# Kernel optimization log

Hardware: AMD Instinct MI355X
Metric: run time of the kernel (lower is better)

The kernel has to match this reference:

```python
import jax, jax.numpy as jnp
import numpy as np
from functools import partial

VOCAB, EMB = 32000, 512
HIDDEN = (1024, 512, 256)
OUT = 7
S, T = 1024, 64  # S = scan (seq) axis, T = 'timesteps' (effective batch)


def _lstm_layer(x, Wih, Whh, bih, bhh):
    """PyTorch-semantics LSTM over axis 0. x: (S, B, E) -> hs: (S, B, H)."""
    B = x.shape[1]
    H = Whh.shape[1]
    # precompute input contribution to all gates: (S, B, 4H)
    xg = jnp.einsum('sbe,ge->sbg', x, Wih) + bih + bhh

    def step(carry, xg_t):
        h, c = carry
        gates = xg_t + h @ Whh.T  # (B, 4H)
        i, f, g, o = jnp.split(gates, 4, axis=-1)  # torch gate order i,f,g,o
        i = jax.nn.sigmoid(i)
        f = jax.nn.sigmoid(f)
        g = jnp.tanh(g)
        o = jax.nn.sigmoid(o)
        c = f * c + i * g
        h = o * jnp.tanh(c)
        return (h, c), h

    init = (jnp.zeros((B, H), x.dtype), jnp.zeros((B, H), x.dtype))
    _, hs = jax.lax.scan(step, init, xg)
    return hs


def setup_inputs():
    key = jax.random.key(0)
    ks = jax.random.split(key, 16)
    inp = {
        'tokens': jax.random.randint(ks[0], (S, T), 0, VOCAB),
        'emb': jax.random.normal(ks[1], (VOCAB, EMB), jnp.float32) * 0.02,
    }
    dims = [(EMB, HIDDEN[0]), (HIDDEN[0], HIDDEN[1]), (HIDDEN[1], HIDDEN[2])]
    for li, (e, h) in enumerate(dims):
        s = 1.0 / np.sqrt(h)
        inp[f'Wih{li}'] = jax.random.uniform(ks[2 + 4 * li], (4 * h, e), jnp.float32, -s, s)
        inp[f'Whh{li}'] = jax.random.uniform(ks[3 + 4 * li], (4 * h, h), jnp.float32, -s, s)
        inp[f'bih{li}'] = jax.random.uniform(ks[4 + 4 * li], (4 * h,), jnp.float32, -s, s)
        inp[f'bhh{li}'] = jax.random.uniform(ks[5 + 4 * li], (4 * h,), jnp.float32, -s, s)
    s = 1.0 / np.sqrt(HIDDEN[2])
    inp['Wlin'] = jax.random.uniform(ks[14], (OUT, HIDDEN[2]), jnp.float32, -s, s)
    inp['blin'] = jax.random.uniform(ks[15], (OUT,), jnp.float32, -s, s)
    return inp


def reference(tokens, emb, Wih0, Whh0, bih0, bhh0, Wih1, Whh1, bih1, bhh1,
              Wih2, Whh2, bih2, bhh2, Wlin, blin):
    x = emb[tokens]                                  # (S, T, EMB)
    h = _lstm_layer(x, Wih0, Whh0, bih0, bhh0)       # (S, T, 1024)
    h = _lstm_layer(h, Wih1, Whh1, bih1, bhh1)       # (S, T, 512)
    h = _lstm_layer(h, Wih2, Whh2, bih2, bhh2)       # (S, T, 256)
    last = h[:, T - 1, :]                            # out[:, timesteps-1, :]
    out = last @ Wlin.T + blin                       # (S, OUT); dropout is identity in eval
    return out
```

## Files before the change

### kernel.cpp

```cpp
#include <hip/hip_runtime.h>
#include <math.h>

#define SLEN 1024

__device__ __forceinline__ float sigf(float x) { return 1.0f / (1.0f + __expf(-x)); }

__device__ __forceinline__ float agent_ld(const float* p) {
  return __hip_atomic_load(p, __ATOMIC_RELAXED, __HIP_MEMORY_SCOPE_AGENT);
}
__device__ __forceinline__ void agent_st(float* p, float v) {
  __hip_atomic_store(p, v, __ATOMIC_RELAXED, __HIP_MEMORY_SCOPE_AGENT);
}
__device__ __forceinline__ bool is_sent(float f) { return __float_as_uint(f) == 0xFFFFFFFFu; }

__device__ __forceinline__ void pin4(float4& v) {
  asm volatile("" : "+v"(v.x), "+v"(v.y), "+v"(v.z), "+v"(v.w));
}

__global__ void embed_k(const int* __restrict__ tokens, const float* __restrict__ emb,
                        float* __restrict__ x) {
  const int t = blockIdx.x;
  const int tok = tokens[t * 64 + 63];
  const float4 v = ((const float4*)(emb + (size_t)tok * 512))[threadIdx.x];
  ((float4*)(x + (size_t)t * 512))[threadIdx.x] = v;
}

template<int HOUT, int EIN, bool POLL_IN>
__device__ void lstm_role(int ublk,
                          const float* __restrict__ Wih, const float* __restrict__ Whh,
                          const float* __restrict__ bih, const float* __restrict__ bhh,
                          const float* __restrict__ in_hist, float* __restrict__ hout) {
  constexpr int C     = EIN + HOUT;
  constexpr int SLOTS = C / 256;
  constexpr int XQ    = EIN / 4;
  constexpr int EPN   = EIN / 512;
  constexpr int HPN   = (HOUT >= 512) ? (HOUT / 512) : 1;
  constexpr bool HGUARD = (HOUT < 512);

  __shared__ __align__(16) float in_lds[2][C];
  __shared__ float h_g[8];

  const int tid = threadIdx.x;
  const int c   = tid & 63;
  const int w   = tid >> 6;
  const int u0  = ublk * 8;
  const int u   = u0 + w;

  float4 wreg[4][SLOTS];
  #pragma unroll
  for (int g = 0; g < 4; ++g) {
    const size_t grow = (size_t)g * HOUT + (size_t)u;
    const float4* wih4 = (const float4*)(Wih + grow * EIN);
    const float4* whh4 = (const float4*)(Whh + grow * HOUT);
    #pragma unroll
    for (int s = 0; s < SLOTS; ++s) {
      const int c4 = s * 64 + c;
      wreg[g][s] = (c4 < XQ) ? wih4[c4] : whh4[c4 - XQ];
    }
  }
  #pragma unroll
  for (int g = 0; g < 4; ++g)
    #pragma unroll
    for (int s = 0; s < SLOTS; ++s)
      pin4(wreg[g][s]);

  float bg0 = 0.f, bg1 = 0.f, bg2 = 0.f, bg3 = 0.f, cst = 0.f;
  if (c == 0) {
    bg0 = bih[0*HOUT + u] + bhh[0*HOUT + u];
    bg1 = bih[1*HOUT + u] + bhh[1*HOUT + u];
    bg2 = bih[2*HOUT + u] + bhh[2*HOUT + u];
    bg3 = bih[3*HOUT + u] + bhh[3*HOUT + u];
  }

  for (int t = 0; t < SLEN; ++t) {
    float ev[EPN];
    float hv[HPN];
    const float* esrc = in_hist + (size_t)t * EIN + EPN * tid;
    const float* hsrc = hout + (size_t)((t > 0 ? t : 1) - 1) * HOUT + HPN * tid;
    const bool hon   = (!HGUARD) || (tid * HPN < HOUT);
    const bool hneed = (t > 0) && hon;

    if constexpr (POLL_IN) {
      for (;;) {
        bool ok = true;
        #pragma unroll
        for (int i = 0; i < EPN; ++i) ev[i] = agent_ld(esrc + i);
        if (hneed) {
          #pragma unroll
          for (int i = 0; i < HPN; ++i) hv[i] = agent_ld(hsrc + i);
          #pragma unroll
          for (int i = 0; i < HPN; ++i) ok &= !is_sent(hv[i]);
        }
        #pragma unroll
        for (int i = 0; i < EPN; ++i) ok &= !is_sent(ev[i]);
        if (ok) break;
        __builtin_amdgcn_s_sleep(1);
      }
    } else {
      #pragma unroll
      for (int i = 0; i < EPN; ++i) ev[i] = esrc[i];
      if (hneed) {
        for (;;) {
          bool ok = true;
          #pragma unroll
          for (int i = 0; i < HPN; ++i) hv[i] = agent_ld(hsrc + i);
          #pragma unroll
          for (int i = 0; i < HPN; ++i) ok &= !is_sent(hv[i]);
          if (ok) break;
          __builtin_amdgcn_s_sleep(1);
        }
      }
    }

    float* dst = in_lds[t & 1];
    #pragma unroll
    for (int i = 0; i < EPN; ++i) dst[EPN * tid + i] = ev[i];
    if (hon) {
      #pragma unroll
      for (int i = 0; i < HPN; ++i) dst[EIN + HPN * tid + i] = hneed ? hv[i] : 0.0f;
    }
    __syncthreads();

    float a0 = 0.f, a1 = 0.f, a2 = 0.f, a3 = 0.f;
    const float4* iv4 = (const float4*)dst;
    #pragma unroll
    for (int s = 0; s < SLOTS; ++s) {
      const float4 iv = iv4[s * 64 + c];
      a0 += wreg[0][s].x*iv.x + wreg[0][s].y*iv.y + wreg[0][s].z*iv.z + wreg[0][s].w*iv.w;
      a1 += wreg[1][s].x*iv.x + wreg[1][s].y*iv.y + wreg[1][s].z*iv.z + wreg[1][s].w*iv.w;
      a2 += wreg[2][s].x*iv.x + wreg[2][s].y*iv.y + wreg[2][s].z*iv.z + wreg[2][s].w*iv.w;
      a3 += wreg[3][s].x*iv.x + wreg[3][s].y*iv.y + wreg[3][s].z*iv.z + wreg[3][s].w*iv.w;
    }
    #pragma unroll
    for (int off = 32; off > 0; off >>= 1) {
      a0 += __shfl_xor(a0, off);
      a1 += __shfl_xor(a1, off);
      a2 += __shfl_xor(a2, off);
      a3 += __shfl_xor(a3, off);
    }
    if (c == 0) {
      const float I = sigf(a0 + bg0);
      const float F = sigf(a1 + bg1);
      const float G = tanhf(a2 + bg2);
      const float O = sigf(a3 + bg3);
      cst = F * cst + I * G;
      h_g[w] = O * tanhf(cst);
    }
    __syncthreads();
    if (tid < 8) {
      agent_st(hout + (size_t)t * HOUT + u0 + tid, h_g[tid]);
    }
  }
}

__device__ void final_role(int fb, const float* __restrict__ h2,
                           const float* __restrict__ Wlin, const float* __restrict__ blin,
                           float* __restrict__ out) {
  const int tid = threadIdx.x;
  float wl[7];
  #pragma unroll
  for (int o = 0; o < 7; ++o) wl[o] = 0.f;
  if (tid < 256) {
    #pragma unroll
    for (int o = 0; o < 7; ++o) wl[o] = Wlin[o * 256 + tid];
  }
  __shared__ float red[4][7];
  for (int t = fb; t < SLEN; t += 8) {
    float h = 0.0f;
    if (tid < 256) {
      h = agent_ld(h2 + (size_t)t * 256 + tid);
      while (is_sent(h)) {
        __builtin_amdgcn_s_sleep(1);
        h = agent_ld(h2 + (size_t)t * 256 + tid);
      }
    }
    float p[7];
    #pragma unroll
    for (int o = 0; o < 7; ++o) p[o] = h * wl[o];
    #pragma unroll
    for (int off = 32; off > 0; off >>= 1) {
      #pragma unroll
      for (int o = 0; o < 7; ++o) p[o] += __shfl_xor(p[o], off);
    }
    const int w = tid >> 6;
    if (w < 4 && (tid & 63) == 0) {
      #pragma unroll
      for (int o = 0; o < 7; ++o) red[w][o] = p[o];
    }
    __syncthreads();
    if (tid == 0) {
      #pragma unroll
      for (int o = 0; o < 7; ++o)
        out[t * 7 + o] = red[0][o] + red[1][o] + red[2][o] + red[3][o] + blin[o];
    }
    __syncthreads();
  }
}

__global__ __launch_bounds__(512, 2) void pipe_k(
    const float* __restrict__ x,
    const float* __restrict__ Wih0, const float* __restrict__ Whh0,
    const float* __restrict__ bih0, const float* __restrict__ bhh0,
    const float* __restrict__ Wih1, const float* __restrict__ Whh1,
    const float* __restrict__ bih1, const float* __restrict__ bhh1,
    const float* __restrict__ Wih2, const float* __restrict__ Whh2,
    const float* __restrict__ bih2, const float* __restrict__ bhh2,
    const float* __restrict__ Wlin, const float* __restrict__ blin,
    float* __restrict__ h0, float* __restrict__ h1, float* __restrict__ h2,
    float* __restrict__ out) {
  const int b = blockIdx.x;
  if (b < 128) {
    lstm_role<1024, 512, false>(b, Wih0, Whh0, bih0, bhh0, x, h0);
  } else if (b < 192) {
    lstm_role<512, 1024, true>(b - 128, Wih1, Whh1, bih1, bhh1, h0, h1);
  } else if (b < 224) {
    lstm_role<256, 512, true>(b - 192, Wih2, Whh2, bih2, bhh2, h1, h2);
  } else {
    final_role(b - 224, h2, Wlin, blin, out);
  }
}

extern "C" void kernel_launch(void* const* d_in, const int* in_sizes, int n_in,
                              void* d_out, int out_size, void* d_ws, size_t ws_size,
                              hipStream_t stream) {
  const int*   tokens = (const int*)  d_in[0];
  const float* emb  = (const float*)d_in[1];
  const float* Wih0 = (const float*)d_in[2];
  const float* Whh0 = (const float*)d_in[3];
  const float* bih0 = (const float*)d_in[4];
  const float* bhh0 = (const float*)d_in[5];
  const float* Wih1 = (const float*)d_in[6];
  const float* Whh1 = (const float*)d_in[7];
  const float* bih1 = (const float*)d_in[8];
  const float* bhh1 = (const float*)d_in[9];
  const float* Wih2 = (const float*)d_in[10];
  const float* Whh2 = (const float*)d_in[11];
  const float* bih2 = (const float*)d_in[12];
  const float* bhh2 = (const float*)d_in[13];
  const float* Wlin = (const float*)d_in[14];
  const float* blin = (const float*)d_in[15];

  float* x  = (float*)d_ws;
  float* h0 = x  + (size_t)1024 * 512;
  float* h1 = h0 + (size_t)1024 * 1024;
  float* h2 = h1 + (size_t)1024 * 512;

  hipMemsetAsync(h0, 0xFF,
                 ((size_t)1024*1024 + (size_t)1024*512 + (size_t)1024*256) * sizeof(float),
                 stream);
  embed_k<<<1024, 128, 0, stream>>>(tokens, emb, x);
  pipe_k<<<232, 512, 0, stream>>>(x, Wih0, Whh0, bih0, bhh0,
                                  Wih1, Whh1, bih1, bhh1,
                                  Wih2, Whh2, bih2, bhh2,
                                  Wlin, blin, h0, h1, h2, (float*)d_out);
}
```

Before: 2.862 ms.

## Halve block size, give each wave two hidden units with doubled register weights

```diff
diff --git a/kernel.cpp b/kernel.cpp
--- a/kernel.cpp
+++ b/kernel.cpp
@@ -33,9 +33,8 @@
   constexpr int C     = EIN + HOUT;
   constexpr int SLOTS = C / 256;
   constexpr int XQ    = EIN / 4;
-  constexpr int EPN   = EIN / 512;
-  constexpr int HPN   = (HOUT >= 512) ? (HOUT / 512) : 1;
-  constexpr bool HGUARD = (HOUT < 512);
+  constexpr int EPN   = EIN / 256;
+  constexpr int HPN   = HOUT / 256;
 
   __shared__ __align__(16) float in_lds[2][C];
   __shared__ float h_g[8];
@@ -44,32 +43,34 @@
   const int c   = tid & 63;
   const int w   = tid >> 6;
   const int u0  = ublk * 8;
-  const int u   = u0 + w;
-
-  float4 wreg[4][SLOTS];
+
+  float4 wreg[8][SLOTS];
   #pragma unroll
-  for (int g = 0; g < 4; ++g) {
-    const size_t grow = (size_t)g * HOUT + (size_t)u;
-    const float4* wih4 = (const float4*)(Wih + grow * EIN);
-    const float4* whh4 = (const float4*)(Whh + grow * HOUT);
-    #pragma unroll
-    for (int s = 0; s < SLOTS; ++s) {
-      const int c4 = s * 64 + c;
-      wreg[g][s] = (c4 < XQ) ? wih4[c4] : whh4[c4 - XQ];
+  for (int j = 0; j < 2; ++j) {
+    #pragma unroll
+    for (int g = 0; g < 4; ++g) {
+      const size_t grow = (size_t)g * HOUT + (size_t)(u0 + 2 * w + j);
+      const float4* wih4 = (const float4*)(Wih + grow * EIN);
+      const float4* whh4 = (const float4*)(Whh + grow * HOUT);
+      #pragma unroll
+      for (int s = 0; s < SLOTS; ++s) {
+        const int c4 = s * 64 + c;
+        wreg[j * 4 + g][s] = (c4 < XQ) ? wih4[c4] : whh4[c4 - XQ];
+      }
     }
   }
   #pragma unroll
-  for (int g = 0; g < 4; ++g)
+  for (int r = 0; r < 8; ++r)
     #pragma unroll
     for (int s = 0; s < SLOTS; ++s)
-      pin4(wreg[g][s]);
-
-  float bg0 = 0.f, bg1 = 0.f, bg2 = 0.f, bg3 = 0.f, cst = 0.f;
-  if (c == 0) {
-    bg0 = bih[0*HOUT + u] + bhh[0*HOUT + u];
-    bg1 = bih[1*HOUT + u] + bhh[1*HOUT + u];
-    bg2 = bih[2*HOUT + u] + bhh[2*HOUT + u];
-    bg3 = bih[3*HOUT + u] + bhh[3*HOUT + u];
+      pin4(wreg[r][s]);
+
+  float bg[4] = {0.f, 0.f, 0.f, 0.f};
+  float cst = 0.f;
+  if (c < 2) {
+    const int u = u0 + 2 * w + c;
+    #pragma unroll
+    for (int g = 0; g < 4; ++g) bg[g] = bih[g * HOUT + u] + bhh[g * HOUT + u];
   }
 
   for (int t = 0; t < SLEN; ++t) {
@@ -77,8 +78,7 @@
     float hv[HPN];
     const float* esrc = in_hist + (size_t)t * EIN + EPN * tid;
     const float* hsrc = hout + (size_t)((t > 0 ? t : 1) - 1) * HOUT + HPN * tid;
-    const bool hon   = (!HGUARD) || (tid * HPN < HOUT);
-    const bool hneed = (t > 0) && hon;
+    const bool hneed = (t > 0);
 
     if constexpr (POLL_IN) {
       for (;;) {
@@ -115,36 +115,35 @@
     float* dst = in_lds[t & 1];
     #pragma unroll
     for (int i = 0; i < EPN; ++i) dst[EPN * tid + i] = ev[i];
-    if (hon) {
-      #pragma unroll
-      for (int i = 0; i < HPN; ++i) dst[EIN + HPN * tid + i] = hneed ? hv[i] : 0.0f;
-    }
-    __syncthreads();
-
-    float a0 = 0.f, a1 = 0.f, a2 = 0.f, a3 = 0.f;
+    #pragma unroll
+    for (int i = 0; i < HPN; ++i) dst[EIN + HPN * tid + i] = hneed ? hv[i] : 0.0f;
+    __syncthreads();
+
+    float a[8];
+    #pragma unroll
+    for (int r = 0; r < 8; ++r) a[r] = 0.f;
     const float4* iv4 = (const float4*)dst;
     #pragma unroll
     for (int s = 0; s < SLOTS; ++s) {
       const float4 iv = iv4[s * 64 + c];
-      a0 += wreg[0][s].x*iv.x + wreg[0][s].y*iv.y + wreg[0][s].z*iv.z + wreg[0][s].w*iv.w;
-      a1 += wreg[1][s].x*iv.x + wreg[1][s].y*iv.y + wreg[1][s].z*iv.z + wreg[1][s].w*iv.w;
-      a2 += wreg[2][s].x*iv.x + wreg[2][s].y*iv.y + wreg[2][s].z*iv.z + wreg[2][s].w*iv.w;
-      a3 += wreg[3][s].x*iv.x + wreg[3][s].y*iv.y + wreg[3][s].z*iv.z + wreg[3][s].w*iv.w;
-    }
-    #pragma unroll
-    for (int off = 32; off > 0; off >>= 1) {
-      a0 += __shfl_xor(a0, off);
-      a1 += __shfl_xor(a1, off);
-      a2 += __shfl_xor(a2, off);
-      a3 += __shfl_xor(a3, off);
-    }
-    if (c == 0) {
-      const float I = sigf(a0 + bg0);
-      const float F = sigf(a1 + bg1);
-      const float G = tanhf(a2 + bg2);
-      const float O = sigf(a3 + bg3);
+      #pragma unroll
+      for (int r = 0; r < 8; ++r) {
+        a[r] += wreg[r][s].x * iv.x + wreg[r][s].y * iv.y
+              + wreg[r][s].z * iv.z + wreg[r][s].w * iv.w;
+      }
+    }
+    #pragma unroll
+    for (int off = 32; off > 0; off >>= 1)
+      #pragma unroll
+      for (int r = 0; r < 8; ++r) a[r] += __shfl_xor(a[r], off);
+
+    if (c < 2) {
+      const float I = sigf(a[c * 4 + 0] + bg[0]);
+      const float F = sigf(a[c * 4 + 1] + bg[1]);
+      const float G = tanhf(a[c * 4 + 2] + bg[2]);
+      const float O = sigf(a[c * 4 + 3] + bg[3]);
       cst = F * cst + I * G;
-      h_g[w] = O * tanhf(cst);
+      h_g[2 * w + c] = O * tanhf(cst);
     }
     __syncthreads();
     if (tid < 8) {
@@ -159,20 +158,13 @@
   const int tid = threadIdx.x;
   float wl[7];
   #pragma unroll
-  for (int o = 0; o < 7; ++o) wl[o] = 0.f;
-  if (tid < 256) {
-    #pragma unroll
-    for (int o = 0; o < 7; ++o) wl[o] = Wlin[o * 256 + tid];
-  }
+  for (int o = 0; o < 7; ++o) wl[o] = Wlin[o * 256 + tid];
   __shared__ float red[4][7];
   for (int t = fb; t < SLEN; t += 8) {
-    float h = 0.0f;
-    if (tid < 256) {
+    float h = agent_ld(h2 + (size_t)t * 256 + tid);
+    while (is_sent(h)) {
+      __builtin_amdgcn_s_sleep(1);
       h = agent_ld(h2 + (size_t)t * 256 + tid);
-      while (is_sent(h)) {
-        __builtin_amdgcn_s_sleep(1);
-        h = agent_ld(h2 + (size_t)t * 256 + tid);
-      }
     }
     float p[7];
     #pragma unroll
@@ -183,7 +175,7 @@
       for (int o = 0; o < 7; ++o) p[o] += __shfl_xor(p[o], off);
     }
     const int w = tid >> 6;
-    if (w < 4 && (tid & 63) == 0) {
+    if ((tid & 63) == 0) {
       #pragma unroll
       for (int o = 0; o < 7; ++o) red[w][o] = p[o];
     }
@@ -197,7 +189,7 @@
   }
 }
 
-__global__ __launch_bounds__(512, 2) void pipe_k(
+__global__ __launch_bounds__(256, 1) void pipe_k(
     const float* __restrict__ x,
     const float* __restrict__ Wih0, const float* __restrict__ Whh0,
     const float* __restrict__ bih0, const float* __restrict__ bhh0,
@@ -249,7 +241,7 @@
                  ((size_t)1024*1024 + (size_t)1024*512 + (size_t)1024*256) * sizeof(float),
                  stream);
   embed_k<<<1024, 128, 0, stream>>>(tokens, emb, x);
-  pipe_k<<<232, 512, 0, stream>>>(x, Wih0, Whh0, bih0, bhh0,
+  pipe_k<<<232, 256, 0, stream>>>(x, Wih0, Whh0, bih0, bhh0,
                                   Wih1, Whh1, bih1, bhh1,
                                   Wih2, Whh2, bih2, bhh2,
                                   Wlin, blin, h0, h1, h2, (float*)d_out);
```

Result: slower. 3.650 ms (+27.5%).

## Precompute layer-0 input gates in separate kernel, shrink recurrent critical path

Applied to the files above, without the earlier changes.

```diff
diff --git a/kernel.cpp b/kernel.cpp
--- a/kernel.cpp
+++ b/kernel.cpp
@@ -16,16 +16,116 @@
 __device__ __forceinline__ void pin4(float4& v) {
   asm volatile("" : "+v"(v.x), "+v"(v.y), "+v"(v.z), "+v"(v.w));
 }
-
-__global__ void embed_k(const int* __restrict__ tokens, const float* __restrict__ emb,
-                        float* __restrict__ x) {
-  const int t = blockIdx.x;
-  const int tok = tokens[t * 64 + 63];
-  const float4 v = ((const float4*)(emb + (size_t)tok * 512))[threadIdx.x];
-  ((float4*)(x + (size_t)t * 512))[threadIdx.x] = v;
-}
-
-template<int HOUT, int EIN, bool POLL_IN>
+#define DOT4(acc, wv, iv)                                                  \
+  acc += (wv).x * (iv).x + (wv).y * (iv).y + (wv).z * (iv).z + (wv).w * (iv).w
+
+__global__ __launch_bounds__(512, 2) void xg0_k(const int* __restrict__ tokens,
+                                                const float* __restrict__ emb,
+                                                const float* __restrict__ Wih0,
+                                                const float* __restrict__ bih0,
+                                                const float* __restrict__ bhh0,
+                                                float* __restrict__ xg0) {
+  const int tid = threadIdx.x, c = tid & 63, w = tid >> 6;
+  const int ublk = blockIdx.x & 127;
+  const int tpar = blockIdx.x >> 7;
+  const int u = ublk * 8 + w;
+  const float4* emb4 = (const float4*)emb;
+  float4 wr[4][2];
+  float bb[4];
+  #pragma unroll
+  for (int g = 0; g < 4; ++g) {
+    const size_t row = (size_t)g * 1024 + u;
+    const float4* w4 = (const float4*)(Wih0 + row * 512);
+    wr[g][0] = w4[2 * c];
+    wr[g][1] = w4[2 * c + 1];
+    bb[g] = bih0[row] + bhh0[row];
+  }
+  float4* xg4 = (float4*)xg0;
+  for (int t = tpar; t < SLEN; t += 2) {
+    const int tok = tokens[t * 64 + 63];
+    const float4 e0 = emb4[(size_t)tok * 128 + 2 * c];
+    const float4 e1 = emb4[(size_t)tok * 128 + 2 * c + 1];
+    float a[4] = {0.f, 0.f, 0.f, 0.f};
+    #pragma unroll
+    for (int g = 0; g < 4; ++g) { DOT4(a[g], wr[g][0], e0); DOT4(a[g], wr[g][1], e1); }
+    #pragma unroll
+    for (int off = 32; off > 0; off >>= 1)
+      #pragma unroll
+      for (int g = 0; g < 4; ++g) a[g] += __shfl_xor(a[g], off);
+    if (c == 0)
+      xg4[(size_t)t * 1024 + u] =
+          make_float4(a[0] + bb[0], a[1] + bb[1], a[2] + bb[2], a[3] + bb[3]);
+  }
+}
+
+__device__ void l0_role(int ublk, const float* __restrict__ Whh,
+                        const float* __restrict__ xg0, float* __restrict__ hout) {
+  __shared__ __align__(16) float in_lds[2][1024];
+  __shared__ float h_g[8];
+  const int tid = threadIdx.x, c = tid & 63, w = tid >> 6;
+  const int u0 = ublk * 8, u = u0 + w;
+
+  float4 wreg[4][4];
+  #pragma unroll
+  for (int g = 0; g < 4; ++g) {
+    const float4* whh4 = (const float4*)(Whh + ((size_t)g * 1024 + u) * 1024);
+    #pragma unroll
+    for (int s = 0; s < 4; ++s) wreg[g][s] = whh4[s * 64 + c];
+  }
+  const float4* xg4 = (const float4*)xg0;
+  float cst = 0.f;
+
+  for (int t = 0; t < SLEN; ++t) {
+    #pragma unroll
+    for (int g = 0; g < 4; ++g)
+      #pragma unroll
+      for (int s = 0; s < 4; ++s) pin4(wreg[g][s]);
+
+    float4 xgv = make_float4(0.f, 0.f, 0.f, 0.f);
+    if (c == 0) xgv = xg4[(size_t)t * 1024 + u];
+
+    float hv0 = 0.f, hv1 = 0.f;
+    if (t > 0) {
+      const float* hsrc = hout + (size_t)(t - 1) * 1024 + 2 * tid;
+      for (;;) {
+        hv0 = agent_ld(hsrc);
+        hv1 = agent_ld(hsrc + 1);
+        if (!is_sent(hv0) && !is_sent(hv1)) break;
+        __builtin_amdgcn_s_sleep(1);
+      }
+    }
+    float* dst = in_lds[t & 1];
+    dst[2 * tid] = hv0;
+    dst[2 * tid + 1] = hv1;
+    __syncthreads();
+
+    float a[4] = {0.f, 0.f, 0.f, 0.f};
+    const float4* iv4 = (const float4*)dst;
+    #pragma unroll
+    for (int s = 0; s < 4; ++s) {
+      const float4 iv = iv4[s * 64 + c];
+      #pragma unroll
+      for (int g = 0; g < 4; ++g) DOT4(a[g], wreg[g][s], iv);
+    }
+    #pragma unroll
+    for (int off = 32; off > 0; off >>= 1)
+      #pragma unroll
+      for (int g = 0; g < 4; ++g) a[g] += __shfl_xor(a[g], off);
+
+    if (c == 0) {
+      const float I = sigf(a[0] + xgv.x);
+      const float F = sigf(a[1] + xgv.y);
+      const float G = tanhf(a[2] + xgv.z);
+      const float O = sigf(a[3] + xgv.w);
+      cst = F * cst + I * G;
+      h_g[w] = O * tanhf(cst);
+    }
+    __syncthreads();
+    if (tid < 8) agent_st(hout + (size_t)t * 1024 + u0 + tid, h_g[tid]);
+  }
+}
+
+template<int HOUT, int EIN>
 __device__ void lstm_role(int ublk,
                           const float* __restrict__ Wih, const float* __restrict__ Whh,
                           const float* __restrict__ bih, const float* __restrict__ bhh,
@@ -34,17 +134,14 @@
   constexpr int SLOTS = C / 256;
   constexpr int XQ    = EIN / 4;
   constexpr int EPN   = EIN / 512;
-  constexpr int HPN   = (HOUT >= 512) ? (HOUT / 512) : 1;
+  constexpr int HPN   = 1;
   constexpr bool HGUARD = (HOUT < 512);
 
   __shared__ __align__(16) float in_lds[2][C];
   __shared__ float h_g[8];
 
-  const int tid = threadIdx.x;
-  const int c   = tid & 63;
-  const int w   = tid >> 6;
-  const int u0  = ublk * 8;
-  const int u   = u0 + w;
+  const int tid = threadIdx.x, c = tid & 63, w = tid >> 6;
+  const int u0 = ublk * 8, u = u0 + w;
 
   float4 wreg[4][SLOTS];
   #pragma unroll
@@ -58,98 +155,67 @@
       wreg[g][s] = (c4 < XQ) ? wih4[c4] : whh4[c4 - XQ];
     }
   }
-  #pragma unroll
-  for (int g = 0; g < 4; ++g)
-    #pragma unroll
-    for (int s = 0; s < SLOTS; ++s)
-      pin4(wreg[g][s]);
-
-  float bg0 = 0.f, bg1 = 0.f, bg2 = 0.f, bg3 = 0.f, cst = 0.f;
+  float bg[4] = {0.f, 0.f, 0.f, 0.f};
+  float cst = 0.f;
   if (c == 0) {
-    bg0 = bih[0*HOUT + u] + bhh[0*HOUT + u];
-    bg1 = bih[1*HOUT + u] + bhh[1*HOUT + u];
-    bg2 = bih[2*HOUT + u] + bhh[2*HOUT + u];
-    bg3 = bih[3*HOUT + u] + bhh[3*HOUT + u];
+    #pragma unroll
+    for (int g = 0; g < 4; ++g) bg[g] = bih[g * HOUT + u] + bhh[g * HOUT + u];
   }
 
   for (int t = 0; t < SLEN; ++t) {
+    #pragma unroll
+    for (int g = 0; g < 4; ++g)
+      #pragma unroll
+      for (int s = 0; s < SLOTS; ++s) pin4(wreg[g][s]);
+
     float ev[EPN];
-    float hv[HPN];
+    float hv = 0.f;
     const float* esrc = in_hist + (size_t)t * EIN + EPN * tid;
-    const float* hsrc = hout + (size_t)((t > 0 ? t : 1) - 1) * HOUT + HPN * tid;
-    const bool hon   = (!HGUARD) || (tid * HPN < HOUT);
+    const float* hsrc = hout + (size_t)((t > 0 ? t : 1) - 1) * HOUT + tid;
+    const bool hon   = (!HGUARD) || (tid < HOUT);
     const bool hneed = (t > 0) && hon;
 
-    if constexpr (POLL_IN) {
-      for (;;) {
-        bool ok = true;
-        #pragma unroll
-        for (int i = 0; i < EPN; ++i) ev[i] = agent_ld(esrc + i);
-        if (hneed) {
-          #pragma unroll
-          for (int i = 0; i < HPN; ++i) hv[i] = agent_ld(hsrc + i);
-          #pragma unroll
-          for (int i = 0; i < HPN; ++i) ok &= !is_sent(hv[i]);
-        }
-        #pragma unroll
-        for (int i = 0; i < EPN; ++i) ok &= !is_sent(ev[i]);
-        if (ok) break;
-        __builtin_amdgcn_s_sleep(1);
-      }
-    } else {
-      #pragma unroll
-      for (int i = 0; i < EPN; ++i) ev[i] = esrc[i];
-      if (hneed) {
-        for (;;) {
-          bool ok = true;
-          #pragma unroll
-          for (int i = 0; i < HPN; ++i) hv[i] = agent_ld(hsrc + i);
-          #pragma unroll
-          for (int i = 0; i < HPN; ++i) ok &= !is_sent(hv[i]);
-          if (ok) break;
-          __builtin_amdgcn_s_sleep(1);
-        }
-      }
-    }
+    for (;;) {
+      bool ok = true;
+      #pragma unroll
+      for (int i = 0; i < EPN; ++i) ev[i] = agent_ld(esrc + i);
+      if (hneed) { hv = agent_ld(hsrc); ok &= !is_sent(hv); }
+      #pragma unroll
+      for (int i = 0; i < EPN; ++i) ok &= !is_sent(ev[i]);
+      if (ok) break;
+      __builtin_amdgcn_s_sleep(1);
+    }
+    if (!hneed) hv = 0.f;
 
     float* dst = in_lds[t & 1];
     #pragma unroll
     for (int i = 0; i < EPN; ++i) dst[EPN * tid + i] = ev[i];
-    if (hon) {
-      #pragma unroll
-      for (int i = 0; i < HPN; ++i) dst[EIN + HPN * tid + i] = hneed ? hv[i] : 0.0f;
-    }
-    __syncthreads();
-
-    float a0 = 0.f, a1 = 0.f, a2 = 0.f, a3 = 0.f;
+    if (hon) dst[EIN + tid] = hv;
+    __syncthreads();
+
+    float a[4] = {0.f, 0.f, 0.f, 0.f};
     const float4* iv4 = (const float4*)dst;
     #pragma unroll
     for (int s = 0; s < SLOTS; ++s) {
       const float4 iv = iv4[s * 64 + c];
-      a0 += wreg[0][s].x*iv.x + wreg[0][s].y*iv.y + wreg[0][s].z*iv.z + wreg[0][s].w*iv.w;
-      a1 += wreg[1][s].x*iv.x + wreg[1][s].y*iv.y + wreg[1][s].z*iv.z + wreg[1][s].w*iv.w;
-      a2 += wreg[2][s].x*iv.x + wreg[2][s].y*iv.y + wreg[2][s].z*iv.z + wreg[2][s].w*iv.w;
-      a3 += wreg[3][s].x*iv.x + wreg[3][s].y*iv.y + wreg[3][s].z*iv.z + wreg[3][s].w*iv.w;
-    }
-    #pragma unroll
-    for (int off = 32; off > 0; off >>= 1) {
-      a0 += __shfl_xor(a0, off);
-      a1 += __shfl_xor(a1, off);
-      a2 += __shfl_xor(a2, off);
-      a3 += __shfl_xor(a3, off);
-    }
+      #pragma unroll
+      for (int g = 0; g < 4; ++g) DOT4(a[g], wreg[g][s], iv);
+    }
+    #pragma unroll
+    for (int off = 32; off > 0; off >>= 1)
+      #pragma unroll
+      for (int g = 0; g < 4; ++g) a[g] += __shfl_xor(a[g], off);
+
     if (c == 0) {
-      const float I = sigf(a0 + bg0);
-      const float F = sigf(a1 + bg1);
-      const float G = tanhf(a2 + bg2);
-      const float O = sigf(a3 + bg3);
+      const float I = sigf(a[0] + bg[0]);
+      const float F = sigf(a[1] + bg[1]);
+      const float G = tanhf(a[2] + bg[2]);
+      const float O = sigf(a[3] + bg[3]);
       cst = F * cst + I * G;
       h_g[w] = O * tanhf(cst);
     }
     __syncthreads();
-    if (tid < 8) {
-      agent_st(hout + (size_t)t * HOUT + u0 + tid, h_g[tid]);
-    }
+    if (tid < 8) agent_st(hout + (size_t)t * HOUT + u0 + tid, h_g[tid]);
   }
 }
 
@@ -197,10 +263,10 @@
   }
 }
 
-__global__ __launch_bounds__(512, 2) void pipe_k(
-    const float* __restrict__ x,
-    const float* __restrict__ Wih0, const float* __restrict__ Whh0,
-    const float* __restrict__ bih0, const float* __restrict__ bhh0,
+__global__ __attribute__((amdgpu_flat_work_group_size(512, 512),
+                          amdgpu_waves_per_eu(2, 2))) void pipe_k(
+    const float* __restrict__ xg0,
+    const float* __restrict__ Whh0,
     const float* __restrict__ Wih1, const float* __restrict__ Whh1,
     const float* __restrict__ bih1, const float* __restrict__ bhh1,
     const float* __restrict__ Wih2, const float* __restrict__ Whh2,
@@ -210,11 +276,11 @@
     float* __restrict__ out) {
   const int b = blockIdx.x;
   if (b < 128) {
-    lstm_role<1024, 512, false>(b, Wih0, Whh0, bih0, bhh0, x, h0);
+    l0_role(b, Whh0, xg0, h0);
   } else if (b < 192) {
-    lstm_role<512, 1024, true>(b - 128, Wih1, Whh1, bih1, bhh1, h0, h1);
+    lstm_role<512, 1024>(b - 128, Wih1, Whh1, bih1, bhh1, h0, h1);
   } else if (b < 224) {
-    lstm_role<256, 512, true>(b - 192, Wih2, Whh2, bih2, bhh2, h1, h2);
+    lstm_role<256, 512>(b - 192, Wih2, Whh2, bih2, bhh2, h1, h2);
   } else {
     final_role(b - 224, h2, Wlin, blin, out);
   }
@@ -240,16 +306,17 @@
   const float* Wlin = (const float*)d_in[14];
   const float* blin = (const float*)d_in[15];
 
-  float* x  = (float*)d_ws;
-  float* h0 = x  + (size_t)1024 * 512;
-  float* h1 = h0 + (size_t)1024 * 1024;
-  float* h2 = h1 + (size_t)1024 * 512;
+  float* xg0 = (float*)d_ws;
+  float* h0  = xg0 + (size_t)1024 * 4096;
+  float* h1  = h0 + (size_t)1024 * 1024;
+  float* h2  = h1 + (size_t)1024 * 512;
 
   hipMemsetAsync(h0, 0xFF,
-                 ((size_t)1024*1024 + (size_t)1024*512 + (size_t)1024*256) * sizeof(float),
+                 ((size_t)1024 * 1024 + (size_t)1024 * 512 + (size_t)1024 * 256) *
+                     sizeof(float),
                  stream);
-  embed_k<<<1024, 128, 0, stream>>>(tokens, emb, x);
-  pipe_k<<<232, 512, 0, stream>>>(x, Wih0, Whh0, bih0, bhh0,
+  xg0_k<<<256, 512, 0, stream>>>(tokens, emb, Wih0, bih0, bhh0, xg0);
+  pipe_k<<<232, 512, 0, stream>>>(xg0, Whh0,
                                   Wih1, Whh1, bih1, bhh1,
                                   Wih2, Whh2, bih2, bhh2,
                                   Wlin, blin, h0, h1, h2, (float*)d_out);
```

Result: slower. 3.100 ms (+8.3%).
